# Performance work log

Measured on AMD Instinct MI355X. Metric: run time of the kernel, lower is better.

The kernel has to match this reference:

```python
import jax, jax.numpy as jnp
import numpy as np

BATCH, LENGTH, DIM = 8, 32768, 256
MAX_N_PEAKS = 400


def _make_meta():
    # deterministic per-sample peak counts in [300, 391]
    n_peaks = 300 + (np.arange(BATCH) * 13) % 101  # [300,313,...,391]
    chunk_sizes = []
    for k in n_peaks:
        base = LENGTH // (k + 1)  # guarantees trailing remainder >= base >= 1
        alt = np.where(np.arange(k) % 2 == 0, 1, -1)
        if k % 2 == 1:
            alt[-1] = 0
        sizes = base + alt  # per-peak chunk lengths, all >= 1
        trailing = LENGTH - int(sizes.sum())  # discarded padding chunk
        assert trailing >= 1
        chunk_sizes.append(np.concatenate([sizes, [trailing]]))
    chunk_size = np.concatenate(chunk_sizes).astype(np.int64)  # (total_chunks,)
    assert chunk_size.sum() == BATCH * LENGTH
    return n_peaks.astype(np.int64), chunk_size


def setup_inputs() -> dict:
    key = jax.random.key(0)
    n_peaks, chunk_size = _make_meta()
    x = jax.random.normal(key, (BATCH, LENGTH, DIM), dtype=jnp.float32)
    return {
        "x": x,
        "chunk_size": jnp.asarray(chunk_size),
        "n_peaks": jnp.asarray(n_peaks),
        "max_n_peaks": MAX_N_PEAKS,
    }


def reference(x, chunk_size, n_peaks, max_n_peaks):
    # x: (B, L, D); chunk_size: (total_chunks,) summing to B*L;
    # each sample owns n_peaks[i]+1 consecutive chunks, last one discarded.
    batch, length, dim = x.shape
    total_chunks = chunk_size.shape[0]
    flat = x.reshape(-1, dim)  # (B*L, D)
    # segment id per flattened position (static output length -> jit friendly)
    seg = jnp.repeat(jnp.arange(total_chunks), chunk_size,
                     total_repeat_length=batch * length)
    # pool_method='sum' -> segmented sum over each chunk
    sums = jax.ops.segment_sum(flat, seg, num_segments=total_chunks)  # (TC, D)
    # first chunk index of each sample
    starts = jnp.concatenate([jnp.zeros(1, dtype=n_peaks.dtype),
                              jnp.cumsum(n_peaks + 1)[:-1]])  # (B,)
    j = jnp.arange(max_n_peaks)  # (P,)
    idx = starts[:, None] + j[None, :]              # (B, P) chunk index per slot
    mask = j[None, :] < n_peaks[:, None]            # valid-peak mask
    idx = jnp.minimum(idx, total_chunks - 1)        # clamp masked-out slots
    out = jnp.where(mask[:, :, None], sums[idx], jnp.zeros((), x.dtype))
    return out  # (B, max_n_peaks, D)
```

## Files before the change

### kernel.cpp

```cpp
#include <hip/hip_runtime.h>

#define DIM 256

__global__ __launch_bounds__(256) void splitpool_kernel(
    const float* __restrict__ x,
    const int* __restrict__ chunk_size,
    const int* __restrict__ n_peaks,
    float* __restrict__ out,
    int B, int L, int P)
{
    const int blk = blockIdx.x;
    const int b   = blk / P;
    const int j   = blk % P;
    const int tid = threadIdx.x;

    float4* out4 = (float4*)(out + (size_t)blk * DIM);

    const int np = n_peaks[b];
    if (j >= np) {
        if (tid < DIM / 4) out4[tid] = make_float4(0.f, 0.f, 0.f, 0.f);
        return;
    }

    int c0 = 0;
    for (int bb = 0; bb < b; ++bb) c0 += n_peaks[bb] + 1;

    __shared__ int ired[256];
    int partial = 0;
    for (int k = tid; k < j; k += 256) partial += chunk_size[c0 + k];
    ired[tid] = partial;
    __syncthreads();
    #pragma unroll
    for (int s = 128; s > 0; s >>= 1) {
        if (tid < s) ired[tid] += ired[tid + s];
        __syncthreads();
    }
    const int prefix = ired[0];
    const int nrows  = chunk_size[c0 + j];
    const size_t row0 = (size_t)b * (size_t)L + (size_t)prefix;

    const int wave = tid >> 6;
    const int lane = tid & 63;
    const float4* xp = (const float4*)(x + row0 * DIM) + lane;

    float4 acc = make_float4(0.f, 0.f, 0.f, 0.f);
    for (int r = wave; r < nrows; r += 4) {
        float4 v = xp[(size_t)r * (DIM / 4)];
        acc.x += v.x; acc.y += v.y; acc.z += v.z; acc.w += v.w;
    }

    __shared__ float4 fred[256];
    fred[tid] = acc;
    __syncthreads();
    if (tid < 64) {
        float4 a  = fred[tid];
        float4 b1 = fred[tid + 64];
        float4 c  = fred[tid + 128];
        float4 d  = fred[tid + 192];
        a.x += b1.x + c.x + d.x;
        a.y += b1.y + c.y + d.y;
        a.z += b1.z + c.z + d.z;
        a.w += b1.w + c.w + d.w;
        out4[tid] = a;
    }
}

extern "C" void kernel_launch(void* const* d_in, const int* in_sizes, int n_in,
                              void* d_out, int out_size, void* d_ws, size_t ws_size,
                              hipStream_t stream) {
    const float* x  = (const float*)d_in[0];
    const int*   cs = (const int*)d_in[1];
    const int*   np = (const int*)d_in[2];
    float*       out = (float*)d_out;

    const int B = in_sizes[2];
    const int P = out_size / (B * DIM);
    const int L = in_sizes[0] / (B * DIM);

    dim3 grid(B * P);
    splitpool_kernel<<<grid, 256, 0, stream>>>(x, cs, np, out, B, L, P);
}
```

Measured before the change: 46.55 us.

## Precompute chunk offsets in a separate scan kernel and unroll row accumulation

Adds a per-sample scan kernel that computes each slot's starting row and row count once, so the pooling blocks no longer each redo a prefix reduction over chunk sizes with shared-memory syncs. The pooling loop is also unrolled by two with independent accumulators to keep more loads in flight. The cost is an extra kernel launch and workspace use, and a fallback path is kept for when the workspace is too small. The scan assumes n_peaks is at most 512 and row offsets fit in int.

```diff
diff --git a/kernel.cpp b/kernel.cpp
--- a/kernel.cpp
+++ b/kernel.cpp
@@ -2,7 +2,92 @@
 
 #define DIM 256
 
+__global__ __launch_bounds__(512) void scan_kernel(
+    const int* __restrict__ chunk_size,
+    const int* __restrict__ n_peaks,
+    int* __restrict__ row0s,
+    int* __restrict__ nrowss,
+    int B, int L, int P)
+{
+    const int b = blockIdx.x;
+    const int t = threadIdx.x;
+
+    const int np = n_peaks[b];
+    int c0 = 0;
+    for (int bb = 0; bb < b; ++bb) c0 += n_peaks[bb] + 1;
+
+    __shared__ int s[512];
+    const int v = (t < np) ? chunk_size[c0 + t] : 0;
+    s[t] = v;
+    __syncthreads();
+    for (int off = 1; off < 512; off <<= 1) {
+        int tv = (t >= off) ? s[t - off] : 0;
+        __syncthreads();
+        s[t] += tv;
+        __syncthreads();
+    }
+    if (t < P) {
+        const bool valid = t < np;
+        const int excl = (t == 0) ? 0 : s[t - 1];
+        row0s[b * P + t]  = valid ? (b * L + excl) : -1;
+        nrowss[b * P + t] = valid ? v : 0;
+    }
+}
+
 __global__ __launch_bounds__(256) void splitpool_kernel(
+    const float* __restrict__ x,
+    const int* __restrict__ row0s,
+    const int* __restrict__ nrowss,
+    float* __restrict__ out)
+{
+    const int blk = blockIdx.x;
+    const int tid = threadIdx.x;
+
+    float4* out4 = (float4*)(out + (size_t)blk * DIM);
+
+    const int row0 = row0s[blk];
+    if (row0 < 0) {
+        if (tid < DIM / 4) out4[tid] = make_float4(0.f, 0.f, 0.f, 0.f);
+        return;
+    }
+    const int nrows = nrowss[blk];
+
+    const int wave = tid >> 6;
+    const int lane = tid & 63;
+    const float4* xp = (const float4*)x + (size_t)row0 * (DIM / 4) + lane;
+
+    float4 a0 = make_float4(0.f, 0.f, 0.f, 0.f);
+    float4 a1 = make_float4(0.f, 0.f, 0.f, 0.f);
+    int r = wave;
+    for (; r + 4 < nrows; r += 8) {
+        float4 v0 = xp[(size_t)r * (DIM / 4)];
+        float4 v1 = xp[(size_t)(r + 4) * (DIM / 4)];
+        a0.x += v0.x; a0.y += v0.y; a0.z += v0.z; a0.w += v0.w;
+        a1.x += v1.x; a1.y += v1.y; a1.z += v1.z; a1.w += v1.w;
+    }
+    if (r < nrows) {
+        float4 v0 = xp[(size_t)r * (DIM / 4)];
+        a0.x += v0.x; a0.y += v0.y; a0.z += v0.z; a0.w += v0.w;
+    }
+    a0.x += a1.x; a0.y += a1.y; a0.z += a1.z; a0.w += a1.w;
+
+    __shared__ float4 fred[256];
+    fred[tid] = a0;
+    __syncthreads();
+    if (tid < 64) {
+        float4 a  = fred[tid];
+        float4 b1 = fred[tid + 64];
+        float4 c  = fred[tid + 128];
+        float4 d  = fred[tid + 192];
+        a.x += b1.x + c.x + d.x;
+        a.y += b1.y + c.y + d.y;
+        a.z += b1.z + c.z + d.z;
+        a.w += b1.w + c.w + d.w;
+        out4[tid] = a;
+    }
+}
+
+__global__ __launch_bounds__(256) void splitpool_fallback(
     const float* __restrict__ x,
     const int* __restrict__ chunk_size,
     const int* __restrict__ n_peaks,
@@ -21,7 +106,6 @@
         if (tid < DIM / 4) out4[tid] = make_float4(0.f, 0.f, 0.f, 0.f);
         return;
     }
-
     int c0 = 0;
     for (int bb = 0; bb < b; ++bb) c0 += n_peaks[bb] + 1;
 
@@ -48,7 +132,6 @@
         float4 v = xp[(size_t)r * (DIM / 4)];
         acc.x += v.x; acc.y += v.y; acc.z += v.z; acc.w += v.w;
     }
-
     __shared__ float4 fred[256];
     fred[tid] = acc;
     __syncthreads();
@@ -76,7 +159,14 @@
     const int B = in_sizes[2];
     const int P = out_size / (B * DIM);
     const int L = in_sizes[0] / (B * DIM);
+    const int slots = B * P;
 
-    dim3 grid(B * P);
-    splitpool_kernel<<<grid, 256, 0, stream>>>(x, cs, np, out, B, L, P);
+    if (ws_size >= (size_t)(2 * slots) * sizeof(int)) {
+        int* row0s  = (int*)d_ws;
+        int* nrowss = row0s + slots;
+        scan_kernel<<<dim3(B), 512, 0, stream>>>(cs, np, row0s, nrowss, B, L, P);
+        splitpool_kernel<<<dim3(slots), 256, 0, stream>>>(x, row0s, nrowss, out);
+    } else {
+        splitpool_fallback<<<dim3(slots), 256, 0, stream>>>(x, cs, np, out, B, L, P);
+    }
 }
```

Result: slower. 49.96 us (+7.3%).

## Assign one wavefront per output slot with shuffle prefix and unrolled row loads

Applied to the files above, without the earlier changes.

Each 64-lane wavefront now handles one (batch, peak) slot instead of a whole 256-thread block. The chunk-size prefix sum uses wave shuffles instead of a shared-memory tree reduction with barriers. The row accumulation is unrolled by four with independent accumulators to keep more loads in flight. This removes the shared-memory reductions and syncthreads and quadruples the slot density per block. In exchange, each slot's rows are now read by a single wave rather than split across four, so per-slot latency may grow.

```diff
diff --git a/kernel.cpp b/kernel.cpp
--- a/kernel.cpp
+++ b/kernel.cpp
@@ -2,67 +2,71 @@
 
 #define DIM 256
 
-__global__ __launch_bounds__(256) void splitpool_kernel(
+__global__ __launch_bounds__(256) void splitpool_wave_kernel(
     const float* __restrict__ x,
     const int* __restrict__ chunk_size,
     const int* __restrict__ n_peaks,
     float* __restrict__ out,
-    int B, int L, int P)
+    int B, int L, int P, int slots)
 {
-    const int blk = blockIdx.x;
-    const int b   = blk / P;
-    const int j   = blk % P;
-    const int tid = threadIdx.x;
+    const int tid  = threadIdx.x;
+    const int wave = tid >> 6;
+    const int lane = tid & 63;
+    const int slot = blockIdx.x * 4 + wave;
+    if (slot >= slots) return;
 
-    float4* out4 = (float4*)(out + (size_t)blk * DIM);
+    const int b = slot / P;
+    const int j = slot - b * P;
+
+    float4* out4 = (float4*)out + (size_t)slot * (DIM / 4) + lane;
 
     const int np = n_peaks[b];
     if (j >= np) {
-        if (tid < DIM / 4) out4[tid] = make_float4(0.f, 0.f, 0.f, 0.f);
+        *out4 = make_float4(0.f, 0.f, 0.f, 0.f);
         return;
     }
 
     int c0 = 0;
     for (int bb = 0; bb < b; ++bb) c0 += n_peaks[bb] + 1;
 
-    __shared__ int ired[256];
     int partial = 0;
-    for (int k = tid; k < j; k += 256) partial += chunk_size[c0 + k];
-    ired[tid] = partial;
-    __syncthreads();
+    for (int k = lane; k < j; k += 64) partial += chunk_size[c0 + k];
     #pragma unroll
-    for (int s = 128; s > 0; s >>= 1) {
-        if (tid < s) ired[tid] += ired[tid + s];
-        __syncthreads();
+    for (int m = 32; m >= 1; m >>= 1) partial += __shfl_xor(partial, m, 64);
+    const int prefix = partial;
+    const int nrows  = chunk_size[c0 + j];
+
+    const float4* xp = (const float4*)x
+                     + ((size_t)b * (size_t)L + (size_t)prefix) * (DIM / 4)
+                     + lane;
+
+    float4 a0 = make_float4(0.f, 0.f, 0.f, 0.f);
+    float4 a1 = make_float4(0.f, 0.f, 0.f, 0.f);
+    float4 a2 = make_float4(0.f, 0.f, 0.f, 0.f);
+    float4 a3 = make_float4(0.f, 0.f, 0.f, 0.f);
+
+    int r = 0;
+    for (; r + 3 < nrows; r += 4) {
+        float4 v0 = xp[(size_t)(r + 0) * (DIM / 4)];
+        float4 v1 = xp[(size_t)(r + 1) * (DIM / 4)];
+        float4 v2 = xp[(size_t)(r + 2) * (DIM / 4)];
+        float4 v3 = xp[(size_t)(r + 3) * (DIM / 4)];
+        a0.x += v0.x; a0.y += v0.y; a0.z += v0.z; a0.w += v0.w;
+        a1.x += v1.x; a1.y += v1.y; a1.z += v1.z; a1.w += v1.w;
+        a2.x += v2.x; a2.y += v2.y; a2.z += v2.z; a2.w += v2.w;
+        a3.x += v3.x; a3.y += v3.y; a3.z += v3.z; a3.w += v3.w;
     }
-    const int prefix = ired[0];
-    const int nrows  = chunk_size[c0 + j];
-    const size_t row0 = (size_t)b * (size_t)L + (size_t)prefix;
-
-    const int wave = tid >> 6;
-    const int lane = tid & 63;
-    const float4* xp = (const float4*)(x + row0 * DIM) + lane;
-
-    float4 acc = make_float4(0.f, 0.f, 0.f, 0.f);
-    for (int r = wave; r < nrows; r += 4) {
-        float4 v = xp[(size_t)r * (DIM / 4)];
-        acc.x += v.x; acc.y += v.y; acc.z += v.z; acc.w += v.w;
+    for (; r < nrows; ++r) {
+        float4 v0 = xp[(size_t)r * (DIM / 4)];
+        a0.x += v0.x; a0.y += v0.y; a0.z += v0.z; a0.w += v0.w;
     }
 
-    __shared__ float4 fred[256];
-    fred[tid] = acc;
-    __syncthreads();
-    if (tid < 64) {
-        float4 a  = fred[tid];
-        float4 b1 = fred[tid + 64];
-        float4 c  = fred[tid + 128];
-        float4 d  = fred[tid + 192];
-        a.x += b1.x + c.x + d.x;
-        a.y += b1.y + c.y + d.y;
-        a.z += b1.z + c.z + d.z;
-        a.w += b1.w + c.w + d.w;
-        out4[tid] = a;
-    }
+    a0.x += a1.x + a2.x + a3.x;
+    a0.y += a1.y + a2.y + a3.y;
+    a0.z += a1.z + a2.z + a3.z;
+    a0.w += a1.w + a2.w + a3.w;
+
+    *out4 = a0;
 }
 
 extern "C" void kernel_launch(void* const* d_in, const int* in_sizes, int n_in,
@@ -76,7 +80,9 @@
     const int B = in_sizes[2];
     const int P = out_size / (B * DIM);
     const int L = in_sizes[0] / (B * DIM);
+    const int slots = B * P;
 
-    dim3 grid(B * P);
-    splitpool_kernel<<<grid, 256, 0, stream>>>(x, cs, np, out, B, L, P);
+    const int blocks = (slots + 3) / 4;
+    splitpool_wave_kernel<<<dim3(blocks), 256, 0, stream>>>(
+        x, cs, np, out, B, L, P, slots);
 }
```

New measurement: 48.11 us. +3.4%, slower.
